# Optimization experiments

Hardware: AMD Instinct MI355X
Metric: run time of the kernel (lower is better)

## Reference

```python
import jax, jax.numpy as jnp
import numpy as np

VOC_SIZE = 40
VOC_EMB = 32
LAYERS = [512, 1024, 2048]
LATENT = 512
START_TOK = 39
STOP_TOK = 0
MAX_STEPS = 50
BATCH = 64


def _gru_cell(x, h, Kg, bg, Kc, bc):
    # TF-style GRU: gates = sigmoid([x,h]@Kg + bg) -> (r, z);
    # cand = tanh([x, r*h]@Kc + bc); h' = z*h + (1-z)*cand
    out = h.shape[-1]
    v = jax.nn.sigmoid(jnp.concatenate([x, h], axis=-1) @ Kg + bg)
    r, z = v[..., :out], v[..., out:]
    c = jnp.tanh(jnp.concatenate([x, r * h], axis=-1) @ Kc + bc)
    return z * h + (1.0 - z) * c


def setup_inputs() -> dict:
    key = jax.random.key(0)
    ks = jax.random.split(key, 16)
    s = 0.05
    inp = {
        'input_vecs': jax.random.normal(ks[0], (BATCH, LATENT), jnp.float32),
        'emb': jax.random.normal(ks[1], (VOC_SIZE, VOC_EMB), jnp.float32) * s,
        'dense_W': jax.random.normal(ks[2], (LATENT, sum(LAYERS)), jnp.float32) * s,
        'dense_b': jnp.zeros((sum(LAYERS),), jnp.float32),
        'dec_W': jax.random.normal(ks[3], (LAYERS[2], VOC_SIZE), jnp.float32) * s,
    }
    ins = [VOC_EMB, LAYERS[0], LAYERS[1]]
    for i in range(3):
        ci = ins[i] + LAYERS[i]
        inp[f'Kg{i}'] = jax.random.normal(ks[4 + 4 * i], (ci, 2 * LAYERS[i]), jnp.float32) * s
        inp[f'bg{i}'] = jnp.ones((2 * LAYERS[i],), jnp.float32)  # TF GRU gate bias init 1.0
        inp[f'Kc{i}'] = jax.random.normal(ks[5 + 4 * i], (ci, LAYERS[i]), jnp.float32) * s
        inp[f'bc{i}'] = jnp.zeros((LAYERS[i],), jnp.float32)
    return inp


def reference(input_vecs, emb, dense_W, dense_b, dec_W,
              Kg0, bg0, Kc0, bc0, Kg1, bg1, Kc1, bc1, Kg2, bg2, Kc2, bc2):
    y = input_vecs @ dense_W + dense_b                       # [B, 3584]
    h0 = y[:, :LAYERS[0]]
    h1 = y[:, LAYERS[0]:LAYERS[0] + LAYERS[1]]
    h2 = y[:, LAYERS[0] + LAYERS[1]:]
    B = input_vecs.shape[0]
    x0 = jnp.broadcast_to(emb[START_TOK], (B, VOC_EMB))      # <s> embedding
    done0 = jnp.zeros((B,), bool)

    def step(carry, _):
        x, h0, h1, h2, done = carry
        n0 = _gru_cell(x, h0, Kg0, bg0, Kc0, bc0)
        n1 = _gru_cell(n0, h1, Kg1, bg1, Kc1, bc1)
        n2 = _gru_cell(n1, h2, Kg2, bg2, Kc2, bc2)
        logits = n2 @ dec_W                                  # [B, 40]
        idx = jnp.argmax(logits, axis=-1)                    # greedy sample
        d = done[:, None]
        # freeze state & outputs once a sequence emitted the stop token
        h0 = jnp.where(d, h0, n0)
        h1 = jnp.where(d, h1, n1)
        h2 = jnp.where(d, h2, n2)
        logits = jnp.where(d, 0.0, logits)
        tok = jnp.where(done, STOP_TOK, idx)
        x = jnp.where(d, x, emb[idx])
        done = done | (idx == STOP_TOK)
        return (x, h0, h1, h2, done), (tok, logits)

    _, (toks, logits) = jax.lax.scan(step, (x0, h0, h1, h2, done0), None, length=MAX_STEPS)
    # toks: [T, B] -> [B, T]; logits: [T, B, V] -> [B, T, V]
    return jnp.transpose(toks).astype(jnp.int32), jnp.transpose(logits, (1, 0, 2))
```

## Files before the change

kernel.cpp:

```cpp
#include <hip/hip_runtime.h>
#include <math.h>

#define NBLK 256
#define TPB  512
#define KB   128
#define ATS  65
#define WTS  36
#define LDSF 12928

#define GC 0
#define GG 512
#define RC 1024
#define RG 1056
#define AB 1088
__device__ unsigned g_sync[1120];
__device__ int g_tok[64];
__device__ int g_done[64];
__device__ __attribute__((aligned(16))) float g_hA[64 * 3584];
__device__ __attribute__((aligned(16))) float g_hB[64 * 3584];
__device__ __attribute__((aligned(16))) float g_v0h[64 * 1024];
__device__ __attribute__((aligned(16))) float g_v1[64 * 2048];
__device__ __attribute__((aligned(16))) float g_c1x[64 * 1024];
__device__ __attribute__((aligned(16))) float g_v2[64 * 4096];
__device__ __attribute__((aligned(16))) float g_c2x[64 * 2048];
__device__ __attribute__((aligned(16))) float g_ekg[40 * 1024];
__device__ __attribute__((aligned(16))) float g_ekc[40 * 512];

__device__ __forceinline__ float sigf(float x) { return 1.0f / (1.0f + __expf(-x)); }
__device__ __forceinline__ float tanhf_(float x) {
  float ax = fabsf(x);
  float e  = __expf(-2.0f * ax);
  float r  = (1.0f - e) / (1.0f + e);
  return copysignf(r, x);
}

__device__ __forceinline__ unsigned armw(unsigned* p, unsigned v) {
  return __hip_atomic_fetch_add(p, v, __ATOMIC_RELAXED, __HIP_MEMORY_SCOPE_AGENT);
}

struct AccP {
  const float* p; int lda;
  __device__ __forceinline__ float4 ld(int r, int k) const {
    return *(const float4*)(p + (size_t)r * lda + k);
  }
};
struct AccH {
  const float* pn; const float* po; int off; int cut;
  __device__ __forceinline__ float4 ld(int r, int k) const {
    const float* b = (k < cut) ? pn : po;
    return *(const float4*)(b + (size_t)r * 3584 + off + k);
  }
};
struct AccRH0 {
  const float* v; const float* ek; const int* tk; const float* h;
  __device__ __forceinline__ float4 ld(int r, int k) const {
    int t = tk[r];
    float4 a  = *(const float4*)(v + (size_t)r * 1024 + k);
    float4 b  = *(const float4*)(ek + (size_t)t * 1024 + k);
    float4 hh = *(const float4*)(h + (size_t)r * 3584 + k);
    return make_float4(sigf(a.x + b.x) * hh.x, sigf(a.y + b.y) * hh.y,
                       sigf(a.z + b.z) * hh.z, sigf(a.w + b.w) * hh.w);
  }
};
struct AccRH {
  const float* v; int ldv; const float* h;
  __device__ __forceinline__ float4 ld(int r, int k) const {
    float4 a  = *(const float4*)(v + (size_t)r * ldv + k);
    float4 hh = *(const float4*)(h + (size_t)r * 3584 + k);
    return make_float4(sigf(a.x) * hh.x, sigf(a.y) * hh.y,
                       sigf(a.z) * hh.z, sigf(a.w) * hh.w);
  }
};

#define FMA8(J, AJ) \
  acc[J][0] = fmaf(AJ, wv0.x, acc[J][0]); acc[J][1] = fmaf(AJ, wv0.y, acc[J][1]); \
  acc[J][2] = fmaf(AJ, wv0.z, acc[J][2]); acc[J][3] = fmaf(AJ, wv0.w, acc[J][3]); \
  acc[J][4] = fmaf(AJ, wv1.x, acc[J][4]); acc[J][5] = fmaf(AJ, wv1.y, acc[J][5]); \
  acc[J][6] = fmaf(AJ, wv1.z, acc[J][6]); acc[J][7] = fmaf(AJ, wv1.w, acc[J][7]);

template <class AF, class EF>
__device__ __forceinline__ void gemm32(const AF& A, const float* __restrict__ W,
                                       const int ldw, const int c0, const int K,
                                       float* __restrict__ lds, const EF& epi) {
  float* AT = lds;
  float* WT = lds + KB * ATS;
  const int tid  = threadIdx.x;
  const int w    = tid >> 6;
  const int lane = tid & 63;
  const int rgrp = lane & 15;
  const int cg   = lane >> 4;
  const int sr = tid >> 3;
  const int sk = (tid & 7) * 16;
  const int wr = tid >> 2;
  const int wc = (tid & 3) * 8;

  float acc[4][8];
#pragma unroll
  for (int j = 0; j < 4; ++j)
#pragma unroll
    for (int e = 0; e < 8; ++e) acc[j][e] = 0.0f;

  float4 aR0, aR1, aR2, aR3, wR0, wR1;
  aR0 = A.ld(sr, sk + 0);  aR1 = A.ld(sr, sk + 4);
  aR2 = A.ld(sr, sk + 8);  aR3 = A.ld(sr, sk + 12);
  {
    const float* wp = W + (size_t)wr * ldw + c0 + wc;
    wR0 = *(const float4*)(wp); wR1 = *(const float4*)(wp + 4);
  }
  const int NT = K / KB;
  for (int t = 0; t < NT; ++t) {
    __syncthreads();
#pragma unroll
    for (int u = 0; u < 4; ++u) {
      float x = (u == 0) ? aR0.x : (u == 1) ? aR1.x : (u == 2) ? aR2.x : aR3.x;
      float y = (u == 0) ? aR0.y : (u == 1) ? aR1.y : (u == 2) ? aR2.y : aR3.y;
      float z = (u == 0) ? aR0.z : (u == 1) ? aR1.z : (u == 2) ? aR2.z : aR3.z;
      float q = (u == 0) ? aR0.w : (u == 1) ? aR1.w : (u == 2) ? aR2.w : aR3.w;
      AT[(sk + 4 * u + 0) * ATS + sr] = x;
      AT[(sk + 4 * u + 1) * ATS + sr] = y;
      AT[(sk + 4 * u + 2) * ATS + sr] = z;
      AT[(sk + 4 * u + 3) * ATS + sr] = q;
    }
    *(float4*)&WT[wr * WTS + wc]     = wR0;
    *(float4*)&WT[wr * WTS + wc + 4] = wR1;
    if (t + 1 < NT) {
      const int kb2 = (t + 1) * KB;
      aR0 = A.ld(sr, kb2 + sk + 0);  aR1 = A.ld(sr, kb2 + sk + 4);
      aR2 = A.ld(sr, kb2 + sk + 8);  aR3 = A.ld(sr, kb2 + sk + 12);
      const float* wp = W + (size_t)(kb2 + wr) * ldw + c0 + wc;
      wR0 = *(const float4*)(wp); wR1 = *(const float4*)(wp + 4);
    }
    __syncthreads();
#pragma unroll
    for (int i = 0; i < KB / 8; ++i) {
      const int kt = i * 8 + w;
      const float a0 = AT[kt * ATS + rgrp * 4 + 0];
      const float a1 = AT[kt * ATS + rgrp * 4 + 1];
      const float a2 = AT[kt * ATS + rgrp * 4 + 2];
      const float a3 = AT[kt * ATS + rgrp * 4 + 3];
      const float4 wv0 = *(const float4*)&WT[kt * WTS + cg * 8];
      const float4 wv1 = *(const float4*)&WT[kt * WTS + cg * 8 + 4];
      FMA8(0, a0) FMA8(1, a1) FMA8(2, a2) FMA8(3, a3)
    }
  }
  float* red = lds;
  const int rb = (rgrp * 4) * 33 + cg * 8;
#define RED_STORE(S) { float* rp = red + (S) * 2112 + rb; \
  _Pragma("unroll") for (int j = 0; j < 4; ++j) _Pragma("unroll") \
    for (int e = 0; e < 8; ++e) rp[j * 33 + e] = acc[j][e]; }
#define RED_ADD(S) { float* rp = red + (S) * 2112 + rb; \
  _Pragma("unroll") for (int j = 0; j < 4; ++j) _Pragma("unroll") \
    for (int e = 0; e < 8; ++e) acc[j][e] += rp[j * 33 + e]; }
  __syncthreads();
  if (w >= 4) RED_STORE(w - 4);
  __syncthreads();
  if (w < 4) RED_ADD(w);
  __syncthreads();
  if (w == 2 || w == 3) RED_STORE(w - 2);
  __syncthreads();
  if (w < 2) RED_ADD(w);
  __syncthreads();
  if (w == 1) RED_STORE(0);
  __syncthreads();
  if (w == 0) {
    RED_ADD(0);
#pragma unroll
    for (int j = 0; j < 4; ++j)
#pragma unroll
      for (int e = 0; e < 8; ++e)
        epi(rgrp * 4 + j, c0 + cg * 8 + e, acc[j][e]);
  }
#undef RED_STORE
#undef RED_ADD
}

__global__ void __launch_bounds__(TPB, 2) decoder_kernel(
    const float* __restrict__ input_vecs, const float* __restrict__ emb,
    const float* __restrict__ dense_W, const float* __restrict__ dense_b,
    const float* __restrict__ dec_W,
    const float* __restrict__ Kg0, const float* __restrict__ bg0,
    const float* __restrict__ Kc0, const float* __restrict__ bc0,
    const float* __restrict__ Kg1, const float* __restrict__ bg1,
    const float* __restrict__ Kc1, const float* __restrict__ bc1,
    const float* __restrict__ Kg2, const float* __restrict__ bg2,
    const float* __restrict__ Kc2, const float* __restrict__ bc2,
    float* __restrict__ out) {
  __shared__ float lds[LDSF];
  __shared__ float lg[40];
  const int bid = blockIdx.x;
  const int tid = threadIdx.x;
  const int grp = bid >> 4;

  unsigned epoch = 0, gbase = 0, rbase = 0;
  if (tid == 0) {
    gbase = armw(&g_sync[GG + grp * 32], 0u);
    rbase = armw(&g_sync[RG], 0u);
  }
  auto gbar = [&]() {
    __syncthreads();
    if (tid == 0) {
      __builtin_amdgcn_fence(__ATOMIC_RELEASE, "agent");
      ++epoch;
      unsigned a = armw(&g_sync[GC + grp * 32], 1u) + 1u;
      if ((a & 15u) == 0u) {
        unsigned r = armw(&g_sync[RC], 1u) + 1u;
        if ((r & 15u) == 0u) armw(&g_sync[RG], 1u);
        unsigned polls = 0;
        while ((int)(armw(&g_sync[RG], 0u) - rbase) < (int)epoch) {
          __builtin_amdgcn_s_sleep(8);
          if ((++polls & 255u) == 0u) {
            if (polls > (1u << 20)) { armw(&g_sync[AB], 1u); break; }
            if (armw(&g_sync[AB], 0u) != 0u) break;
          }
        }
        armw(&g_sync[GG + grp * 32], 1u);
      } else {
        unsigned polls = 0;
        while ((int)(armw(&g_sync[GG + grp * 32], 0u) - gbase) < (int)epoch) {
          __builtin_amdgcn_s_sleep(8);
          if ((++polls & 255u) == 0u) {
            if (polls > (1u << 20)) { armw(&g_sync[AB], 1u); break; }
            if (armw(&g_sync[AB], 0u) != 0u) break;
          }
        }
      }
    }
    __syncthreads();
    __builtin_amdgcn_fence(__ATOMIC_ACQUIRE, "agent");
  };

  if (bid < 112) {
    AccP A{input_vecs, 512};
    auto epi = [&](int r, int c, float v) { g_hA[(size_t)r * 3584 + c] = v + dense_b[c]; };
    gemm32(A, dense_W, 3584, bid * 32, 512, lds, epi);
  }
  if (bid >= NBLK - 32) {
    int base = (bid - (NBLK - 32)) * 1920;
    for (int o = base + tid; o < base + 1920; o += TPB) {
      if (o < 40960) {
        int r = o >> 10, c = o & 1023;
        float s = 0.0f;
        for (int k = 0; k < 32; ++k) s += emb[r * 32 + k] * Kg0[k * 1024 + c];
        g_ekg[o] = s;
      } else {
        int o2 = o - 40960;
        int r = o2 >> 9, c = o2 & 511;
        float s = 0.0f;
        for (int k = 0; k < 32; ++k) s += emb[r * 32 + k] * Kc0[k * 512 + c];
        g_ekc[o2] = s;
      }
    }
  }
  if (bid == 128 && tid < 64) { g_tok[tid] = 39; g_done[tid] = 0; }
  gbar();

  if (bid < 32) {
    AccH A{g_hA, g_hA, 0, 512};
    auto epi = [&](int r, int c, float v) { g_v0h[r * 1024 + c] = v + bg0[c]; };
    gemm32(A, Kg0 + 32 * 1024, 1024, bid * 32, 512, lds, epi);
  }
  gbar();

  for (int t = 0; t < 50; ++t) {
    const float* hOld = (t & 1) ? g_hB : g_hA;
    float*       hNew = (t & 1) ? g_hA : g_hB;

    if (bid < 16) {
      AccRH0 A{g_v0h, g_ekg, g_tok, hOld};
      auto epi = [&](int r, int c, float v) {
        int tk = g_tok[r];
        float cx = g_ekc[tk * 512 + c] + bc0[c];
        float z  = sigf(g_v0h[r * 1024 + 512 + c] + g_ekg[tk * 1024 + 512 + c]);
        float ho = hOld[(size_t)r * 3584 + c];
        hNew[(size_t)r * 3584 + c] = z * ho + (1.0f - z) * tanhf_(v + cx);
      };
      gemm32(A, Kc0 + 32 * 512, 512, bid * 32, 512, lds, epi);
    }
    gbar();

    if (bid < 96) {
      AccH A{hNew, hOld, 0, 512};
      if (bid < 64) {
        auto epi = [&](int r, int c, float v) { g_v1[r * 2048 + c] = v + bg1[c]; };
        gemm32(A, Kg1, 2048, bid * 32, 1536, lds, epi);
      } else {
        auto epi = [&](int r, int c, float v) { g_c1x[r * 1024 + c] = v + bc1[c]; };
        gemm32(A, Kc1, 1024, (bid - 64) * 32, 512, lds, epi);
      }
    }
    gbar();

    if (bid < 32) {
      AccRH A{g_v1, 2048, hOld + 512};
      auto epi = [&](int r, int c, float v) {
        float z  = sigf(g_v1[r * 2048 + 1024 + c]);
        float cx = g_c1x[r * 1024 + c];
        float ho = hOld[(size_t)r * 3584 + 512 + c];
        hNew[(size_t)r * 3584 + 512 + c] = z * ho + (1.0f - z) * tanhf_(v + cx);
      };
      gemm32(A, Kc1 + 512 * 1024, 1024, bid * 32, 1024, lds, epi);
    }
    gbar();

    if (bid < 192) {
      AccH A{hNew, hOld, 512, 1024};
      if (bid < 128) {
        auto epi = [&](int r, int c, float v) { g_v2[r * 4096 + c] = v + bg2[c]; };
        gemm32(A, Kg2, 4096, bid * 32, 3072, lds, epi);
      } else {
        auto epi = [&](int r, int c, float v) { g_c2x[r * 2048 + c] = v + bc2[c]; };
        gemm32(A, Kc2, 2048, (bid - 128) * 32, 1024, lds, epi);
      }
    }
    gbar();

    if (bid < 64) {
      AccRH A{g_v2, 4096, hOld + 1536};
      auto epi = [&](int r, int c, float v) {
        float z  = sigf(g_v2[r * 4096 + 2048 + c]);
        float cx = g_c2x[r * 2048 + c];
        float ho = hOld[(size_t)r * 3584 + 1536 + c];
        hNew[(size_t)r * 3584 + 1536 + c] = z * ho + (1.0f - z) * tanhf_(v + cx);
      };
      gemm32(A, Kc2 + 1024 * 2048, 2048, bid * 32, 2048, lds, epi);
    }
    gbar();

    if (bid < 64) {
      const int b = bid;
      float acc = 0.0f;
      if (tid < 320) {
        const int v = tid >> 3, p = tid & 7;
        for (int i = 0; i < 64; ++i) {
          const int k = p * 4 + i * 32;
          float4 h = *(const float4*)(hNew + (size_t)b * 3584 + 1536 + k);
          acc += h.x * dec_W[k * 40 + v] + h.y * dec_W[(k + 1) * 40 + v] +
                 h.z * dec_W[(k + 2) * 40 + v] + h.w * dec_W[(k + 3) * 40 + v];
        }
        acc += __shfl_xor(acc, 4);
        acc += __shfl_xor(acc, 2);
        acc += __shfl_xor(acc, 1);
        if (p == 0) lg[v] = acc;
      }
      __syncthreads();
      if (tid == 0) {
        int idx = 0; float best = lg[0];
        for (int v = 1; v < 40; ++v) { if (lg[v] > best) { best = lg[v]; idx = v; } }
        const int dn = g_done[b];
        out[b * 50 + t] = dn ? 0.0f : (float)idx;
        float* olg = out + 3200 + (size_t)(b * 50 + t) * 40;
        for (int v = 0; v < 40; ++v) olg[v] = dn ? 0.0f : lg[v];
        if (!dn) { g_tok[b] = idx; if (idx == 0) g_done[b] = 1; }
      }
    } else if (bid < 96) {
      AccH A{hNew, hOld, 0, 512};
      auto epi = [&](int r, int c, float v) { g_v0h[r * 1024 + c] = v + bg0[c]; };
      gemm32(A, Kg0 + 32 * 1024, 1024, (bid - 64) * 32, 512, lds, epi);
    }
    gbar();
  }
}

extern "C" void kernel_launch(void* const* d_in, const int* in_sizes, int n_in,
                              void* d_out, int out_size, void* d_ws, size_t ws_size,
                              hipStream_t stream) {
  (void)in_sizes; (void)n_in; (void)d_ws; (void)ws_size; (void)out_size;
  void* p0  = d_in[0];  void* p1  = d_in[1];  void* p2  = d_in[2];
  void* p3  = d_in[3];  void* p4  = d_in[4];  void* p5  = d_in[5];
  void* p6  = d_in[6];  void* p7  = d_in[7];  void* p8  = d_in[8];
  void* p9  = d_in[9];  void* p10 = d_in[10]; void* p11 = d_in[11];
  void* p12 = d_in[12]; void* p13 = d_in[13]; void* p14 = d_in[14];
  void* p15 = d_in[15]; void* p16 = d_in[16]; void* po  = d_out;
  void* args[] = {&p0, &p1, &p2, &p3, &p4, &p5, &p6, &p7, &p8,
                  &p9, &p10, &p11, &p12, &p13, &p14, &p15, &p16, &po};
  hipLaunchCooperativeKernel((const void*)decoder_kernel, dim3(NBLK), dim3(TPB),
                             args, 0, stream);
}
```

Measured before the change: 20.33 ms.

## Split-K the GRU gate GEMMs across more blocks and stream weights directly from global memory

The layer-1 and layer-2 gate GEMMs are split along K into two halves written to separate buffers, and the partial sums are added where they are consumed. This spreads each phase over more of the 256 persistent blocks. The layer-2 candidate GEMM is also split in half, and its GRU update is fused into the decoder phase. Separately, the GEMM inner loop no longer stages weights in LDS: each thread reads its weight row straight from global memory with a one-step register prefetch, and A is read as a float4. The aims are to shorten the serial per-step phases and to cut LDS traffic and barriers. In exchange the code writes and reads extra partial-sum buffers and has less latency hiding on the weight loads.

```diff
diff --git a/kernel.cpp b/kernel.cpp
--- a/kernel.cpp
+++ b/kernel.cpp
@@ -5,8 +5,7 @@
 #define TPB  512
 #define KB   128
 #define ATS  65
-#define WTS  36
-#define LDSF 12928
+#define LDSF 8448
 
 #define GC 0
 #define GG 512
@@ -19,9 +18,13 @@
 __device__ __attribute__((aligned(16))) float g_hA[64 * 3584];
 __device__ __attribute__((aligned(16))) float g_hB[64 * 3584];
 __device__ __attribute__((aligned(16))) float g_v0h[64 * 1024];
-__device__ __attribute__((aligned(16))) float g_v1[64 * 2048];
+__device__ __attribute__((aligned(16))) float g_v1a[64 * 2048];
+__device__ __attribute__((aligned(16))) float g_v1b[64 * 2048];
 __device__ __attribute__((aligned(16))) float g_c1x[64 * 1024];
-__device__ __attribute__((aligned(16))) float g_v2[64 * 4096];
+__device__ __attribute__((aligned(16))) float g_v2a[64 * 4096];
+__device__ __attribute__((aligned(16))) float g_v2b[64 * 4096];
+__device__ __attribute__((aligned(16))) float g_cnd2a[64 * 2048];
+__device__ __attribute__((aligned(16))) float g_cnd2b[64 * 2048];
 __device__ __attribute__((aligned(16))) float g_c2x[64 * 2048];
 __device__ __attribute__((aligned(16))) float g_ekg[40 * 1024];
 __device__ __attribute__((aligned(16))) float g_ekc[40 * 512];
@@ -62,14 +65,29 @@
                        sigf(a.z + b.z) * hh.z, sigf(a.w + b.w) * hh.w);
   }
 };
-struct AccRH {
-  const float* v; int ldv; const float* h;
+struct AccR1 {
+  const float* va; const float* vb; const float* h;
   __device__ __forceinline__ float4 ld(int r, int k) const {
-    float4 a  = *(const float4*)(v + (size_t)r * ldv + k);
+    float4 a  = *(const float4*)(va + (size_t)r * 2048 + k);
+    float4 b  = *(const float4*)(vb + (size_t)r * 2048 + k);
     float4 hh = *(const float4*)(h + (size_t)r * 3584 + k);
-    return make_float4(sigf(a.x) * hh.x, sigf(a.y) * hh.y,
-                       sigf(a.z) * hh.z, sigf(a.w) * hh.w);
-  }
+    return make_float4(sigf(a.x + b.x) * hh.x, sigf(a.y + b.y) * hh.y,
+                       sigf(a.z + b.z) * hh.z, sigf(a.w + b.w) * hh.w);
+  }
+};
+struct AccR2 {
+  const float* va; const float* vb; const float* h;
+  __device__ __forceinline__ float4 ld(int r, int k) const {
+    float4 a  = *(const float4*)(va + (size_t)r * 4096 + k);
+    float4 b  = *(const float4*)(vb + (size_t)r * 4096 + k);
+    float4 hh = *(const float4*)(h + (size_t)r * 3584 + k);
+    return make_float4(sigf(a.x + b.x) * hh.x, sigf(a.y + b.y) * hh.y,
+                       sigf(a.z + b.z) * hh.z, sigf(a.w + b.w) * hh.w);
+  }
+};
+template <class Inner> struct AccOff {
+  Inner in; int base;
+  __device__ __forceinline__ float4 ld(int r, int k) const { return in.ld(r, base + k); }
 };
 
 #define FMA8(J, AJ) \
@@ -83,7 +101,6 @@
                                        const int ldw, const int c0, const int K,
                                        float* __restrict__ lds, const EF& epi) {
   float* AT = lds;
-  float* WT = lds + KB * ATS;
   const int tid  = threadIdx.x;
   const int w    = tid >> 6;
   const int lane = tid & 63;
@@ -91,8 +108,6 @@
   const int cg   = lane >> 4;
   const int sr = tid >> 3;
   const int sk = (tid & 7) * 16;
-  const int wr = tid >> 2;
-  const int wc = (tid & 3) * 8;
 
   float acc[4][8];
 #pragma unroll
@@ -100,47 +115,43 @@
 #pragma unroll
     for (int e = 0; e < 8; ++e) acc[j][e] = 0.0f;
 
-  float4 aR0, aR1, aR2, aR3, wR0, wR1;
-  aR0 = A.ld(sr, sk + 0);  aR1 = A.ld(sr, sk + 4);
-  aR2 = A.ld(sr, sk + 8);  aR3 = A.ld(sr, sk + 12);
-  {
-    const float* wp = W + (size_t)wr * ldw + c0 + wc;
-    wR0 = *(const float4*)(wp); wR1 = *(const float4*)(wp + 4);
-  }
+  float4 aR0 = A.ld(sr, sk + 0), aR1 = A.ld(sr, sk + 4);
+  float4 aR2 = A.ld(sr, sk + 8), aR3 = A.ld(sr, sk + 12);
+
   const int NT = K / KB;
+  const float* wbase = W + (size_t)w * ldw + c0 + cg * 8;
+
   for (int t = 0; t < NT; ++t) {
     __syncthreads();
-#pragma unroll
-    for (int u = 0; u < 4; ++u) {
-      float x = (u == 0) ? aR0.x : (u == 1) ? aR1.x : (u == 2) ? aR2.x : aR3.x;
-      float y = (u == 0) ? aR0.y : (u == 1) ? aR1.y : (u == 2) ? aR2.y : aR3.y;
-      float z = (u == 0) ? aR0.z : (u == 1) ? aR1.z : (u == 2) ? aR2.z : aR3.z;
-      float q = (u == 0) ? aR0.w : (u == 1) ? aR1.w : (u == 2) ? aR2.w : aR3.w;
-      AT[(sk + 4 * u + 0) * ATS + sr] = x;
-      AT[(sk + 4 * u + 1) * ATS + sr] = y;
-      AT[(sk + 4 * u + 2) * ATS + sr] = z;
-      AT[(sk + 4 * u + 3) * ATS + sr] = q;
-    }
-    *(float4*)&WT[wr * WTS + wc]     = wR0;
-    *(float4*)&WT[wr * WTS + wc + 4] = wR1;
+    AT[(sk + 0)  * ATS + sr] = aR0.x;  AT[(sk + 1)  * ATS + sr] = aR0.y;
+    AT[(sk + 2)  * ATS + sr] = aR0.z;  AT[(sk + 3)  * ATS + sr] = aR0.w;
+    AT[(sk + 4)  * ATS + sr] = aR1.x;  AT[(sk + 5)  * ATS + sr] = aR1.y;
+    AT[(sk + 6)  * ATS + sr] = aR1.z;  AT[(sk + 7)  * ATS + sr] = aR1.w;
+    AT[(sk + 8)  * ATS + sr] = aR2.x;  AT[(sk + 9)  * ATS + sr] = aR2.y;
+    AT[(sk + 10) * ATS + sr] = aR2.z;  AT[(sk + 11) * ATS + sr] = aR2.w;
+    AT[(sk + 12) * ATS + sr] = aR3.x;  AT[(sk + 13) * ATS + sr] = aR3.y;
+    AT[(sk + 14) * ATS + sr] = aR3.z;  AT[(sk + 15) * ATS + sr] = aR3.w;
     if (t + 1 < NT) {
       const int kb2 = (t + 1) * KB;
       aR0 = A.ld(sr, kb2 + sk + 0);  aR1 = A.ld(sr, kb2 + sk + 4);
       aR2 = A.ld(sr, kb2 + sk + 8);  aR3 = A.ld(sr, kb2 + sk + 12);
-      const float* wp = W + (size_t)(kb2 + wr) * ldw + c0 + wc;
-      wR0 = *(const float4*)(wp); wR1 = *(const float4*)(wp + 4);
     }
     __syncthreads();
+    const float* wrow = wbase + (size_t)t * KB * ldw;
+    float4 wv0 = *(const float4*)wrow;
+    float4 wv1 = *(const float4*)(wrow + 4);
 #pragma unroll
     for (int i = 0; i < KB / 8; ++i) {
       const int kt = i * 8 + w;
-      const float a0 = AT[kt * ATS + rgrp * 4 + 0];
-      const float a1 = AT[kt * ATS + rgrp * 4 + 1];
-      const float a2 = AT[kt * ATS + rgrp * 4 + 2];
-      const float a3 = AT[kt * ATS + rgrp * 4 + 3];
-      const float4 wv0 = *(const float4*)&WT[kt * WTS + cg * 8];
-      const float4 wv1 = *(const float4*)&WT[kt * WTS + cg * 8 + 4];
-      FMA8(0, a0) FMA8(1, a1) FMA8(2, a2) FMA8(3, a3)
+      const float4 av = *(const float4*)&AT[kt * ATS + rgrp * 4];
+      float4 nw0 = wv0, nw1 = wv1;
+      if (i + 1 < KB / 8) {
+        wrow += (size_t)8 * ldw;
+        nw0 = *(const float4*)wrow;
+        nw1 = *(const float4*)(wrow + 4);
+      }
+      FMA8(0, av.x) FMA8(1, av.y) FMA8(2, av.z) FMA8(3, av.w)
+      wv0 = nw0; wv1 = nw1;
     }
   }
   float* red = lds;
@@ -255,7 +266,7 @@
   gbar();
 
   if (bid < 32) {
-    AccH A{g_hA, g_hA, 0, 512};
+    AccP A{g_hA, 3584};
     auto epi = [&](int r, int c, float v) { g_v0h[r * 1024 + c] = v + bg0[c]; };
     gemm32(A, Kg0 + 32 * 1024, 1024, bid * 32, 512, lds, epi);
   }
@@ -278,62 +289,88 @@
     }
     gbar();
 
-    if (bid < 96) {
-      AccH A{hNew, hOld, 0, 512};
-      if (bid < 64) {
-        auto epi = [&](int r, int c, float v) { g_v1[r * 2048 + c] = v + bg1[c]; };
-        gemm32(A, Kg1, 2048, bid * 32, 1536, lds, epi);
+    if (bid < 128) {
+      const int half = bid >> 6, ch = bid & 63;
+      AccOff<AccH> A{{hNew, hOld, 0, 512}, half * 768};
+      float* dst = half ? g_v1b : g_v1a;
+      if (half == 0) {
+        auto epi = [&](int r, int c, float v) { dst[r * 2048 + c] = v + bg1[c]; };
+        gemm32(A, Kg1, 2048, ch * 32, 768, lds, epi);
       } else {
-        auto epi = [&](int r, int c, float v) { g_c1x[r * 1024 + c] = v + bc1[c]; };
-        gemm32(A, Kc1, 1024, (bid - 64) * 32, 512, lds, epi);
-      }
+        auto epi = [&](int r, int c, float v) { dst[r * 2048 + c] = v; };
+        gemm32(A, Kg1 + (size_t)768 * 2048, 2048, ch * 32, 768, lds, epi);
+      }
+    } else if (bid < 160) {
+      AccP A{hNew, 3584};
+      auto epi = [&](int r, int c, float v) { g_c1x[r * 1024 + c] = v + bc1[c]; };
+      gemm32(A, Kc1, 1024, (bid - 128) * 32, 512, lds, epi);
     }
     gbar();
 
     if (bid < 32) {
-      AccRH A{g_v1, 2048, hOld + 512};
+      AccR1 A{g_v1a, g_v1b, hOld + 512};
       auto epi = [&](int r, int c, float v) {
-        float z  = sigf(g_v1[r * 2048 + 1024 + c]);
+        float z  = sigf(g_v1a[r * 2048 + 1024 + c] + g_v1b[r * 2048 + 1024 + c]);
         float cx = g_c1x[r * 1024 + c];
         float ho = hOld[(size_t)r * 3584 + 512 + c];
         hNew[(size_t)r * 3584 + 512 + c] = z * ho + (1.0f - z) * tanhf_(v + cx);
       };
-      gemm32(A, Kc1 + 512 * 1024, 1024, bid * 32, 1024, lds, epi);
-    }
-    gbar();
-
-    if (bid < 192) {
-      AccH A{hNew, hOld, 512, 1024};
-      if (bid < 128) {
-        auto epi = [&](int r, int c, float v) { g_v2[r * 4096 + c] = v + bg2[c]; };
-        gemm32(A, Kg2, 4096, bid * 32, 3072, lds, epi);
+      gemm32(A, Kc1 + (size_t)512 * 1024, 1024, bid * 32, 1024, lds, epi);
+    }
+    gbar();
+
+    {
+      const int half = bid >> 7, ch = bid & 127;
+      AccOff<AccH> A{{hNew, hOld, 512, 1024}, half * 1536};
+      if (half == 0) {
+        auto epi = [&](int r, int c, float v) { g_v2a[(size_t)r * 4096 + c] = v + bg2[c]; };
+        gemm32(A, Kg2, 4096, ch * 32, 1536, lds, epi);
       } else {
-        auto epi = [&](int r, int c, float v) { g_c2x[r * 2048 + c] = v + bc2[c]; };
-        gemm32(A, Kc2, 2048, (bid - 128) * 32, 1024, lds, epi);
-      }
-    }
-    gbar();
-
-    if (bid < 64) {
-      AccRH A{g_v2, 4096, hOld + 1536};
-      auto epi = [&](int r, int c, float v) {
-        float z  = sigf(g_v2[r * 4096 + 2048 + c]);
-        float cx = g_c2x[r * 2048 + c];
-        float ho = hOld[(size_t)r * 3584 + 1536 + c];
-        hNew[(size_t)r * 3584 + 1536 + c] = z * ho + (1.0f - z) * tanhf_(v + cx);
-      };
-      gemm32(A, Kc2 + 1024 * 2048, 2048, bid * 32, 2048, lds, epi);
+        auto epi = [&](int r, int c, float v) { g_v2b[(size_t)r * 4096 + c] = v; };
+        gemm32(A, Kg2 + (size_t)1536 * 4096, 4096, ch * 32, 1536, lds, epi);
+      }
+    }
+    gbar();
+
+    if (bid < 128) {
+      const int half = bid >> 6, ch = bid & 63;
+      AccOff<AccR2> A{{g_v2a, g_v2b, hOld + 1536}, half * 1024};
+      float* dst = half ? g_cnd2b : g_cnd2a;
+      auto epi = [&](int r, int c, float v) { dst[r * 2048 + c] = v; };
+      gemm32(A, Kc2 + (size_t)(1024 + half * 1024) * 2048, 2048, ch * 32, 1024, lds, epi);
+    } else if (bid < 192) {
+      AccP A{hNew + 512, 3584};
+      auto epi = [&](int r, int c, float v) { g_c2x[r * 2048 + c] = v + bc2[c]; };
+      gemm32(A, Kc2, 2048, (bid - 128) * 32, 1024, lds, epi);
     }
     gbar();
 
     if (bid < 64) {
       const int b = bid;
+      float* h2row = lds;
+      {
+        const int c = tid * 4;
+        float4 va = *(const float4*)&g_v2a[(size_t)b * 4096 + 2048 + c];
+        float4 vb = *(const float4*)&g_v2b[(size_t)b * 4096 + 2048 + c];
+        float4 ca = *(const float4*)&g_cnd2a[b * 2048 + c];
+        float4 cb = *(const float4*)&g_cnd2b[b * 2048 + c];
+        float4 cx = *(const float4*)&g_c2x[b * 2048 + c];
+        float4 ho = *(const float4*)&hOld[(size_t)b * 3584 + 1536 + c];
+        float4 r;
+#define GRU2(comp) { float z = sigf(va.comp + vb.comp); \
+        r.comp = z * ho.comp + (1.0f - z) * tanhf_(ca.comp + cb.comp + cx.comp); }
+        GRU2(x) GRU2(y) GRU2(z) GRU2(w)
+#undef GRU2
+        *(float4*)&hNew[(size_t)b * 3584 + 1536 + c] = r;
+        *(float4*)&h2row[c] = r;
+      }
+      __syncthreads();
       float acc = 0.0f;
       if (tid < 320) {
         const int v = tid >> 3, p = tid & 7;
         for (int i = 0; i < 64; ++i) {
           const int k = p * 4 + i * 32;
-          float4 h = *(const float4*)(hNew + (size_t)b * 3584 + 1536 + k);
+          float4 h = *(const float4*)&h2row[k];
           acc += h.x * dec_W[k * 40 + v] + h.y * dec_W[(k + 1) * 40 + v] +
                  h.z * dec_W[(k + 2) * 40 + v] + h.w * dec_W[(k + 3) * 40 + v];
         }
@@ -353,7 +390,7 @@
         if (!dn) { g_tok[b] = idx; if (idx == 0) g_done[b] = 1; }
       }
     } else if (bid < 96) {
-      AccH A{hNew, hOld, 0, 512};
+      AccP A{hNew, 3584};
       auto epi = [&](int r, int c, float v) { g_v0h[r * 1024 + c] = v + bg0[c]; };
       gemm32(A, Kg0 + 32 * 1024, 1024, (bid - 64) * 32, 512, lds, epi);
     }
```

After: 19.22 ms. 1.06x faster.

## Rewrite GEMM with transposed activations, readlane weight broadcast, and split-K across blocks

Applied to the files above, without the earlier changes.

Replaces the LDS-tiled 64x32 GEMM with a register-only kernel. Activations are stored transposed ([feature][batch]) so each lane owns one batch row, and weights are broadcast across the wave with readlane. Several gate GEMMs are split along K into two halves spread over more blocks, and the layer-2 GRU combine moves into the logits stage. This removes LDS staging and its syncs and raises parallelism per barrier phase, at the cost of extra partial-sum buffers, dual row/transposed copies, more register use (launch bounds now 1 block per CU) and scattered transposed stores.

```diff
diff --git a/kernel.cpp b/kernel.cpp
--- a/kernel.cpp
+++ b/kernel.cpp
@@ -3,10 +3,8 @@
 
 #define NBLK 256
 #define TPB  512
-#define KB   128
-#define ATS  65
-#define WTS  36
-#define LDSF 12928
+#define RS   33
+#define LDSF (4 * 64 * RS)
 
 #define GC 0
 #define GG 512
@@ -16,13 +14,24 @@
 __device__ unsigned g_sync[1120];
 __device__ int g_tok[64];
 __device__ int g_done[64];
-__device__ __attribute__((aligned(16))) float g_hA[64 * 3584];
-__device__ __attribute__((aligned(16))) float g_hB[64 * 3584];
-__device__ __attribute__((aligned(16))) float g_v0h[64 * 1024];
-__device__ __attribute__((aligned(16))) float g_v1[64 * 2048];
-__device__ __attribute__((aligned(16))) float g_c1x[64 * 1024];
-__device__ __attribute__((aligned(16))) float g_v2[64 * 4096];
-__device__ __attribute__((aligned(16))) float g_c2x[64 * 2048];
+__device__ __attribute__((aligned(16))) float g_hTA[3584 * 64];
+__device__ __attribute__((aligned(16))) float g_hTB[3584 * 64];
+__device__ __attribute__((aligned(16))) float g_hRowA[64 * 2048];
+__device__ __attribute__((aligned(16))) float g_hRowB[64 * 2048];
+__device__ __attribute__((aligned(16))) float g_v0hT[512 * 64];
+__device__ __attribute__((aligned(16))) float g_v0hR[64 * 512];
+__device__ __attribute__((aligned(16))) float g_v1aT[1024 * 64];
+__device__ __attribute__((aligned(16))) float g_v1bT[1024 * 64];
+__device__ __attribute__((aligned(16))) float g_v1aR[64 * 1024];
+__device__ __attribute__((aligned(16))) float g_v1bR[64 * 1024];
+__device__ __attribute__((aligned(16))) float g_c1xR[64 * 1024];
+__device__ __attribute__((aligned(16))) float g_v2aT[2048 * 64];
+__device__ __attribute__((aligned(16))) float g_v2bT[2048 * 64];
+__device__ __attribute__((aligned(16))) float g_v2aR[64 * 2048];
+__device__ __attribute__((aligned(16))) float g_v2bR[64 * 2048];
+__device__ __attribute__((aligned(16))) float g_cn2aR[64 * 2048];
+__device__ __attribute__((aligned(16))) float g_cn2bR[64 * 2048];
+__device__ __attribute__((aligned(16))) float g_c2xR[64 * 2048];
 __device__ __attribute__((aligned(16))) float g_ekg[40 * 1024];
 __device__ __attribute__((aligned(16))) float g_ekc[40 * 512];
 
@@ -33,148 +42,141 @@
   float r  = (1.0f - e) / (1.0f + e);
   return copysignf(r, x);
 }
-
 __device__ __forceinline__ unsigned armw(unsigned* p, unsigned v) {
   return __hip_atomic_fetch_add(p, v, __ATOMIC_RELAXED, __HIP_MEMORY_SCOPE_AGENT);
 }
 
-struct AccP {
+struct F1 { float x; };
+struct F3 { float x, y, z; };
+
+struct ATplain {
+  const float* t; int f0;
+  using P = F1;
+  __device__ __forceinline__ P load(int f, int lane) const {
+    return {t[(size_t)(f0 + f) * 64 + lane]};
+  }
+  __device__ __forceinline__ float eval(P p) const { return p.x; }
+};
+struct ATg {
   const float* p; int lda;
-  __device__ __forceinline__ float4 ld(int r, int k) const {
-    return *(const float4*)(p + (size_t)r * lda + k);
-  }
+  using P = F1;
+  __device__ __forceinline__ P load(int f, int lane) const {
+    return {p[(size_t)lane * lda + f]};
+  }
+  __device__ __forceinline__ float eval(P q) const { return q.x; }
 };
-struct AccH {
-  const float* pn; const float* po; int off; int cut;
-  __device__ __forceinline__ float4 ld(int r, int k) const {
-    const float* b = (k < cut) ? pn : po;
-    return *(const float4*)(b + (size_t)r * 3584 + off + k);
-  }
+struct ATcat {
+  const float* tn; const float* to; int f0; int cut;
+  using P = F1;
+  __device__ __forceinline__ P load(int f, int lane) const {
+    const int fa = f0 + f;
+    const float* b = (fa < cut) ? tn : to;
+    return {b[(size_t)fa * 64 + lane]};
+  }
+  __device__ __forceinline__ float eval(P p) const { return p.x; }
 };
-struct AccRH0 {
-  const float* v; const float* ek; const int* tk; const float* h;
-  __device__ __forceinline__ float4 ld(int r, int k) const {
-    int t = tk[r];
-    float4 a  = *(const float4*)(v + (size_t)r * 1024 + k);
-    float4 b  = *(const float4*)(ek + (size_t)t * 1024 + k);
-    float4 hh = *(const float4*)(h + (size_t)r * 3584 + k);
-    return make_float4(sigf(a.x + b.x) * hh.x, sigf(a.y + b.y) * hh.y,
-                       sigf(a.z + b.z) * hh.z, sigf(a.w + b.w) * hh.w);
-  }
+struct ATr0 {
+  const float* v; const float* ekl; const float* h;
+  using P = F3;
+  __device__ __forceinline__ P load(int f, int lane) const {
+    return {v[(size_t)f * 64 + lane], ekl[f], h[(size_t)f * 64 + lane]};
+  }
+  __device__ __forceinline__ float eval(P p) const { return sigf(p.x + p.y) * p.z; }
 };
-struct AccRH {
-  const float* v; int ldv; const float* h;
-  __device__ __forceinline__ float4 ld(int r, int k) const {
-    float4 a  = *(const float4*)(v + (size_t)r * ldv + k);
-    float4 hh = *(const float4*)(h + (size_t)r * 3584 + k);
-    return make_float4(sigf(a.x) * hh.x, sigf(a.y) * hh.y,
-                       sigf(a.z) * hh.z, sigf(a.w) * hh.w);
-  }
+struct ATr {
+  const float* va; const float* vb; const float* h; int f0; int hf0;
+  using P = F3;
+  __device__ __forceinline__ P load(int f, int lane) const {
+    const size_t fa = (size_t)(f0 + f) * 64 + lane;
+    return {va[fa], vb[fa], h[(size_t)(hf0 + f) * 64 + lane]};
+  }
+  __device__ __forceinline__ float eval(P p) const { return sigf(p.x + p.y) * p.z; }
 };
 
-#define FMA8(J, AJ) \
-  acc[J][0] = fmaf(AJ, wv0.x, acc[J][0]); acc[J][1] = fmaf(AJ, wv0.y, acc[J][1]); \
-  acc[J][2] = fmaf(AJ, wv0.z, acc[J][2]); acc[J][3] = fmaf(AJ, wv0.w, acc[J][3]); \
-  acc[J][4] = fmaf(AJ, wv1.x, acc[J][4]); acc[J][5] = fmaf(AJ, wv1.y, acc[J][5]); \
-  acc[J][6] = fmaf(AJ, wv1.z, acc[J][6]); acc[J][7] = fmaf(AJ, wv1.w, acc[J][7]);
-
 template <class AF, class EF>
-__device__ __forceinline__ void gemm32(const AF& A, const float* __restrict__ W,
-                                       const int ldw, const int c0, const int K,
-                                       float* __restrict__ lds, const EF& epi) {
-  float* AT = lds;
-  float* WT = lds + KB * ATS;
+__device__ __forceinline__ void gemmT(const AF& A, const float* __restrict__ W,
+                                      const int ldw, const int c0, const int K,
+                                      float* __restrict__ lds, const EF& epi) {
   const int tid  = threadIdx.x;
   const int w    = tid >> 6;
   const int lane = tid & 63;
-  const int rgrp = lane & 15;
-  const int cg   = lane >> 4;
-  const int sr = tid >> 3;
-  const int sk = (tid & 7) * 16;
-  const int wr = tid >> 2;
-  const int wc = (tid & 3) * 8;
-
-  float acc[4][8];
-#pragma unroll
-  for (int j = 0; j < 4; ++j)
-#pragma unroll
-    for (int e = 0; e < 8; ++e) acc[j][e] = 0.0f;
-
-  float4 aR0, aR1, aR2, aR3, wR0, wR1;
-  aR0 = A.ld(sr, sk + 0);  aR1 = A.ld(sr, sk + 4);
-  aR2 = A.ld(sr, sk + 8);  aR3 = A.ld(sr, sk + 12);
+  const int S    = K >> 3;
+  const int wcol = c0 + (lane & 31);
+  const int wkh  = (lane >> 5) << 3;
+
+  float acc[32];
+#pragma unroll
+  for (int c = 0; c < 32; ++c) acc[c] = 0.0f;
+
+  typename AF::P aq[8];
+  float wq[4];
+#pragma unroll
+  for (int u = 0; u < 8; ++u) aq[u] = A.load(w + 8 * u, lane);
+#pragma unroll
+  for (int p = 0; p < 4; ++p)
+    wq[p] = W[(size_t)(w + 16 * p + wkh) * ldw + wcol];
+
+#define WFMA(HALF, AV) \
+  _Pragma("unroll") \
+  for (int c = 0; c < 32; ++c) { \
+    const float s_ = __uint_as_float(__builtin_amdgcn_readlane(__float_as_uint(wv), (HALF) + c)); \
+    acc[c] = fmaf(s_, (AV), acc[c]); \
+  }
+
+  int j2 = 0;
+  for (; j2 + 16 <= S; j2 += 8) {
+#pragma unroll
+    for (int u = 0; u < 8; u += 2) {
+      const int p = u >> 1;
+      const float wv = wq[p];
+      const float a0 = A.eval(aq[u]);
+      WFMA(0, a0)
+      aq[u] = A.load(w + 8 * (j2 + u + 8), lane);
+      const float a1 = A.eval(aq[u + 1]);
+      WFMA(32, a1)
+      aq[u + 1] = A.load(w + 8 * (j2 + u + 9), lane);
+      wq[p] = W[(size_t)(w + 8 * (j2 + u + 8) + wkh) * ldw + wcol];
+    }
+  }
   {
-    const float* wp = W + (size_t)wr * ldw + c0 + wc;
-    wR0 = *(const float4*)(wp); wR1 = *(const float4*)(wp + 4);
-  }
-  const int NT = K / KB;
-  for (int t = 0; t < NT; ++t) {
-    __syncthreads();
-#pragma unroll
-    for (int u = 0; u < 4; ++u) {
-      float x = (u == 0) ? aR0.x : (u == 1) ? aR1.x : (u == 2) ? aR2.x : aR3.x;
-      float y = (u == 0) ? aR0.y : (u == 1) ? aR1.y : (u == 2) ? aR2.y : aR3.y;
-      float z = (u == 0) ? aR0.z : (u == 1) ? aR1.z : (u == 2) ? aR2.z : aR3.z;
-      float q = (u == 0) ? aR0.w : (u == 1) ? aR1.w : (u == 2) ? aR2.w : aR3.w;
-      AT[(sk + 4 * u + 0) * ATS + sr] = x;
-      AT[(sk + 4 * u + 1) * ATS + sr] = y;
-      AT[(sk + 4 * u + 2) * ATS + sr] = z;
-      AT[(sk + 4 * u + 3) * ATS + sr] = q;
-    }
-    *(float4*)&WT[wr * WTS + wc]     = wR0;
-    *(float4*)&WT[wr * WTS + wc + 4] = wR1;
-    if (t + 1 < NT) {
-      const int kb2 = (t + 1) * KB;
-      aR0 = A.ld(sr, kb2 + sk + 0);  aR1 = A.ld(sr, kb2 + sk + 4);
-      aR2 = A.ld(sr, kb2 + sk + 8);  aR3 = A.ld(sr, kb2 + sk + 12);
-      const float* wp = W + (size_t)(kb2 + wr) * ldw + c0 + wc;
-      wR0 = *(const float4*)(wp); wR1 = *(const float4*)(wp + 4);
-    }
-    __syncthreads();
-#pragma unroll
-    for (int i = 0; i < KB / 8; ++i) {
-      const int kt = i * 8 + w;
-      const float a0 = AT[kt * ATS + rgrp * 4 + 0];
-      const float a1 = AT[kt * ATS + rgrp * 4 + 1];
-      const float a2 = AT[kt * ATS + rgrp * 4 + 2];
-      const float a3 = AT[kt * ATS + rgrp * 4 + 3];
-      const float4 wv0 = *(const float4*)&WT[kt * WTS + cg * 8];
-      const float4 wv1 = *(const float4*)&WT[kt * WTS + cg * 8 + 4];
-      FMA8(0, a0) FMA8(1, a1) FMA8(2, a2) FMA8(3, a3)
-    }
-  }
+#pragma unroll
+    for (int u = 0; u < 8; u += 2) {
+      const int p = u >> 1;
+      const float wv = wq[p];
+      const float a0 = A.eval(aq[u]);
+      WFMA(0, a0)
+      const float a1 = A.eval(aq[u + 1]);
+      WFMA(32, a1)
+    }
+  }
+#undef WFMA
+
   float* red = lds;
-  const int rb = (rgrp * 4) * 33 + cg * 8;
-#define RED_STORE(S) { float* rp = red + (S) * 2112 + rb; \
-  _Pragma("unroll") for (int j = 0; j < 4; ++j) _Pragma("unroll") \
-    for (int e = 0; e < 8; ++e) rp[j * 33 + e] = acc[j][e]; }
-#define RED_ADD(S) { float* rp = red + (S) * 2112 + rb; \
-  _Pragma("unroll") for (int j = 0; j < 4; ++j) _Pragma("unroll") \
-    for (int e = 0; e < 8; ++e) acc[j][e] += rp[j * 33 + e]; }
-  __syncthreads();
-  if (w >= 4) RED_STORE(w - 4);
-  __syncthreads();
-  if (w < 4) RED_ADD(w);
-  __syncthreads();
-  if (w == 2 || w == 3) RED_STORE(w - 2);
-  __syncthreads();
-  if (w < 2) RED_ADD(w);
-  __syncthreads();
-  if (w == 1) RED_STORE(0);
+#define RST(SL) { float* rp = red + (SL) * (64 * RS) + lane * RS; \
+  _Pragma("unroll") for (int c = 0; c < 32; ++c) rp[c] = acc[c]; }
+#define RAD(SL) { float* rp = red + (SL) * (64 * RS) + lane * RS; \
+  _Pragma("unroll") for (int c = 0; c < 32; ++c) acc[c] += rp[c]; }
+  __syncthreads();
+  if (w >= 4) RST(w - 4);
+  __syncthreads();
+  if (w < 4) RAD(w);
+  __syncthreads();
+  if (w == 2 || w == 3) RST(w - 2);
+  __syncthreads();
+  if (w < 2) RAD(w);
+  __syncthreads();
+  if (w == 1) RST(0);
   __syncthreads();
   if (w == 0) {
-    RED_ADD(0);
-#pragma unroll
-    for (int j = 0; j < 4; ++j)
-#pragma unroll
-      for (int e = 0; e < 8; ++e)
-        epi(rgrp * 4 + j, c0 + cg * 8 + e, acc[j][e]);
-  }
-#undef RED_STORE
-#undef RED_ADD
+    RAD(0);
+#pragma unroll
+    for (int c = 0; c < 32; ++c) epi(lane, c, acc[c]);
+  }
+#undef RST
+#undef RAD
 }
 
-__global__ void __launch_bounds__(TPB, 2) decoder_kernel(
+__global__ void __launch_bounds__(TPB, 1) decoder_kernel(
     const float* __restrict__ input_vecs, const float* __restrict__ emb,
     const float* __restrict__ dense_W, const float* __restrict__ dense_b,
     const float* __restrict__ dec_W,
@@ -230,9 +232,15 @@
   };
 
   if (bid < 112) {
-    AccP A{input_vecs, 512};
-    auto epi = [&](int r, int c, float v) { g_hA[(size_t)r * 3584 + c] = v + dense_b[c]; };
-    gemm32(A, dense_W, 3584, bid * 32, 512, lds, epi);
+    const int c0 = bid * 32;
+    ATg A{input_vecs, 512};
+    auto epi = [&](int r, int c, float v) {
+      const int oc = c0 + c;
+      const float val = v + dense_b[oc];
+      g_hTA[(size_t)oc * 64 + r] = val;
+      if (oc >= 1536) g_hRowA[r * 2048 + oc - 1536] = val;
+    };
+    gemmT(A, dense_W, 3584, c0, 512, lds, epi);
   }
   if (bid >= NBLK - 32) {
     int base = (bid - (NBLK - 32)) * 1920;
@@ -255,85 +263,136 @@
   gbar();
 
   if (bid < 32) {
-    AccH A{g_hA, g_hA, 0, 512};
-    auto epi = [&](int r, int c, float v) { g_v0h[r * 1024 + c] = v + bg0[c]; };
-    gemm32(A, Kg0 + 32 * 1024, 1024, bid * 32, 512, lds, epi);
+    const int c0 = bid * 32;
+    ATplain A{g_hTA, 0};
+    auto epi = [&](int r, int c, float v) {
+      const int oc = c0 + c;
+      const float val = v + bg0[oc];
+      if (oc < 512) g_v0hT[(size_t)oc * 64 + r] = val;
+      else g_v0hR[r * 512 + oc - 512] = val;
+    };
+    gemmT(A, Kg0 + 32 * 1024, 1024, c0, 512, lds, epi);
   }
   gbar();
 
   for (int t = 0; t < 50; ++t) {
-    const float* hOld = (t & 1) ? g_hB : g_hA;
-    float*       hNew = (t & 1) ? g_hA : g_hB;
+    const float* hOldT = (t & 1) ? g_hTB : g_hTA;
+    float*       hNewT = (t & 1) ? g_hTA : g_hTB;
+    const float* hRowOld = (t & 1) ? g_hRowB : g_hRowA;
+    float*       hRowNew = (t & 1) ? g_hRowA : g_hRowB;
 
     if (bid < 16) {
-      AccRH0 A{g_v0h, g_ekg, g_tok, hOld};
-      auto epi = [&](int r, int c, float v) {
-        int tk = g_tok[r];
-        float cx = g_ekc[tk * 512 + c] + bc0[c];
-        float z  = sigf(g_v0h[r * 1024 + 512 + c] + g_ekg[tk * 1024 + 512 + c]);
-        float ho = hOld[(size_t)r * 3584 + c];
-        hNew[(size_t)r * 3584 + c] = z * ho + (1.0f - z) * tanhf_(v + cx);
-      };
-      gemm32(A, Kc0 + 32 * 512, 512, bid * 32, 512, lds, epi);
-    }
-    gbar();
-
-    if (bid < 96) {
-      AccH A{hNew, hOld, 0, 512};
-      if (bid < 64) {
-        auto epi = [&](int r, int c, float v) { g_v1[r * 2048 + c] = v + bg1[c]; };
-        gemm32(A, Kg1, 2048, bid * 32, 1536, lds, epi);
-      } else {
-        auto epi = [&](int r, int c, float v) { g_c1x[r * 1024 + c] = v + bc1[c]; };
-        gemm32(A, Kc1, 1024, (bid - 64) * 32, 512, lds, epi);
-      }
+      const int c0 = bid * 32;
+      const int myTok = g_tok[tid & 63];
+      const float* ekl = g_ekg + (size_t)myTok * 1024;
+      const float* ecl = g_ekc + (size_t)myTok * 512;
+      ATr0 A{g_v0hT, ekl, hOldT};
+      auto epi = [&](int r, int c, float v) {
+        const int oc = c0 + c;
+        const float z  = sigf(g_v0hR[r * 512 + oc] + ekl[512 + oc]);
+        const float cx = ecl[oc] + bc0[oc];
+        const float ho = hOldT[(size_t)oc * 64 + r];
+        hNewT[(size_t)oc * 64 + r] = z * ho + (1.0f - z) * tanhf_(v + cx);
+      };
+      gemmT(A, Kc0 + 32 * 512, 512, c0, 512, lds, epi);
+    }
+    gbar();
+
+    if (bid < 128) {
+      const int half = bid >> 6, ch = bid & 63, c0 = ch * 32;
+      ATcat A{hNewT, hOldT, half * 768, 512};
+      auto epi = [&](int r, int c, float v) {
+        const int oc = c0 + c;
+        const float val = half ? v : v + bg1[oc];
+        if (oc < 1024) (half ? g_v1bT : g_v1aT)[(size_t)oc * 64 + r] = val;
+        else (half ? g_v1bR : g_v1aR)[r * 1024 + oc - 1024] = val;
+      };
+      gemmT(A, Kg1 + (size_t)(half * 768) * 2048, 2048, c0, 768, lds, epi);
+    } else if (bid < 160) {
+      const int c0 = (bid - 128) * 32;
+      ATplain A{hNewT, 0};
+      auto epi = [&](int r, int c, float v) {
+        const int oc = c0 + c;
+        g_c1xR[r * 1024 + oc] = v + bc1[oc];
+      };
+      gemmT(A, Kc1, 1024, c0, 512, lds, epi);
     }
     gbar();
 
     if (bid < 32) {
-      AccRH A{g_v1, 2048, hOld + 512};
-      auto epi = [&](int r, int c, float v) {
-        float z  = sigf(g_v1[r * 2048 + 1024 + c]);
-        float cx = g_c1x[r * 1024 + c];
-        float ho = hOld[(size_t)r * 3584 + 512 + c];
-        hNew[(size_t)r * 3584 + 512 + c] = z * ho + (1.0f - z) * tanhf_(v + cx);
-      };
-      gemm32(A, Kc1 + 512 * 1024, 1024, bid * 32, 1024, lds, epi);
-    }
-    gbar();
-
-    if (bid < 192) {
-      AccH A{hNew, hOld, 512, 1024};
-      if (bid < 128) {
-        auto epi = [&](int r, int c, float v) { g_v2[r * 4096 + c] = v + bg2[c]; };
-        gemm32(A, Kg2, 4096, bid * 32, 3072, lds, epi);
-      } else {
-        auto epi = [&](int r, int c, float v) { g_c2x[r * 2048 + c] = v + bc2[c]; };
-        gemm32(A, Kc2, 2048, (bid - 128) * 32, 1024, lds, epi);
-      }
-    }
-    gbar();
-
-    if (bid < 64) {
-      AccRH A{g_v2, 4096, hOld + 1536};
-      auto epi = [&](int r, int c, float v) {
-        float z  = sigf(g_v2[r * 4096 + 2048 + c]);
-        float cx = g_c2x[r * 2048 + c];
-        float ho = hOld[(size_t)r * 3584 + 1536 + c];
-        hNew[(size_t)r * 3584 + 1536 + c] = z * ho + (1.0f - z) * tanhf_(v + cx);
-      };
-      gemm32(A, Kc2 + 1024 * 2048, 2048, bid * 32, 2048, lds, epi);
+      const int c0 = bid * 32;
+      ATr A{g_v1aT, g_v1bT, hOldT, 0, 512};
+      auto epi = [&](int r, int c, float v) {
+        const int oc = c0 + c;
+        const float z  = sigf(g_v1aR[r * 1024 + oc] + g_v1bR[r * 1024 + oc]);
+        const float cx = g_c1xR[r * 1024 + oc];
+        const float ho = hOldT[(size_t)(512 + oc) * 64 + r];
+        hNewT[(size_t)(512 + oc) * 64 + r] = z * ho + (1.0f - z) * tanhf_(v + cx);
+      };
+      gemmT(A, Kc1 + (size_t)512 * 1024, 1024, c0, 1024, lds, epi);
+    }
+    gbar();
+
+    {
+      const int half = bid >> 7, ch = bid & 127, c0 = ch * 32;
+      ATcat A{hNewT, hOldT, 512 + half * 1536, 1536};
+      auto epi = [&](int r, int c, float v) {
+        const int oc = c0 + c;
+        const float val = half ? v : v + bg2[oc];
+        if (oc < 2048) (half ? g_v2bT : g_v2aT)[(size_t)oc * 64 + r] = val;
+        else (half ? g_v2bR : g_v2aR)[r * 2048 + oc - 2048] = val;
+      };
+      gemmT(A, Kg2 + (size_t)(half * 1536) * 4096, 4096, c0, 1536, lds, epi);
+    }
+    gbar();
+
+    if (bid < 128) {
+      const int half = bid >> 6, ch = bid & 63, c0 = ch * 32;
+      ATr A{g_v2aT, g_v2bT, hOldT, half * 1024, 1536 + half * 1024};
+      float* dst = half ? g_cn2bR : g_cn2aR;
+      auto epi = [&](int r, int c, float v) { dst[r * 2048 + c0 + c] = v; };
+      gemmT(A, Kc2 + (size_t)(1024 + half * 1024) * 2048, 2048, c0, 1024, lds, epi);
+    } else if (bid < 192) {
+      const int c0 = (bid - 128) * 32;
+      ATplain A{hNewT, 512};
+      auto epi = [&](int r, int c, float v) {
+        const int oc = c0 + c;
+        g_c2xR[r * 2048 + oc] = v + bc2[oc];
+      };
+      gemmT(A, Kc2, 2048, c0, 1024, lds, epi);
     }
     gbar();
 
     if (bid < 64) {
       const int b = bid;
+      float* h2row = lds;
+      {
+        const int c = tid * 4;
+        float4 va = *(const float4*)&g_v2aR[b * 2048 + c];
+        float4 vb = *(const float4*)&g_v2bR[b * 2048 + c];
+        float4 ca = *(const float4*)&g_cn2aR[b * 2048 + c];
+        float4 cb = *(const float4*)&g_cn2bR[b * 2048 + c];
+        float4 cx = *(const float4*)&g_c2xR[b * 2048 + c];
+        float4 ho = *(const float4*)&hRowOld[b * 2048 + c];
+        float4 r;
+#define GRU2(comp) { const float z = sigf(va.comp + vb.comp); \
+        r.comp = z * ho.comp + (1.0f - z) * tanhf_(ca.comp + cb.comp + cx.comp); }
+        GRU2(x) GRU2(y) GRU2(z) GRU2(w)
+#undef GRU2
+        *(float4*)&hRowNew[b * 2048 + c] = r;
+        hNewT[(size_t)(1536 + c + 0) * 64 + b] = r.x;
+        hNewT[(size_t)(1536 + c + 1) * 64 + b] = r.y;
+        hNewT[(size_t)(1536 + c + 2) * 64 + b] = r.z;
+        hNewT[(size_t)(1536 + c + 3) * 64 + b] = r.w;
+        *(float4*)&h2row[c] = r;
+      }
+      __syncthreads();
       float acc = 0.0f;
       if (tid < 320) {
         const int v = tid >> 3, p = tid & 7;
         for (int i = 0; i < 64; ++i) {
           const int k = p * 4 + i * 32;
-          float4 h = *(const float4*)(hNew + (size_t)b * 3584 + 1536 + k);
+          float4 h = *(const float4*)&h2row[k];
           acc += h.x * dec_W[k * 40 + v] + h.y * dec_W[(k + 1) * 40 + v] +
                  h.z * dec_W[(k + 2) * 40 + v] + h.w * dec_W[(k + 3) * 40 + v];
         }
@@ -353,9 +412,15 @@
         if (!dn) { g_tok[b] = idx; if (idx == 0) g_done[b] = 1; }
       }
     } else if (bid < 96) {
-      AccH A{hNew, hOld, 0, 512};
-      auto epi = [&](int r, int c, float v) { g_v0h[r * 1024 + c] = v + bg0[c]; };
-      gemm32(A, Kg0 + 32 * 1024, 1024, (bid - 64) * 32, 512, lds, epi);
+      const int c0 = (bid - 64) * 32;
+      ATplain A{hNewT, 0};
+      auto epi = [&](int r, int c, float v) {
+        const int oc = c0 + c;
+        const float val = v + bg0[oc];
+        if (oc < 512) g_v0hT[(size_t)oc * 64 + r] = val;
+        else g_v0hR[r * 512 + oc - 512] = val;
+      };
+      gemmT(A, Kg0 + 32 * 1024, 1024, c0, 512, lds, epi);
     }
     gbar();
   }
```

New measurement: 21.25 ms. 1.05x slower.
